# Kernel optimization log

Hardware: AMD Instinct MI355X
Metric: run time of the kernel (lower is better)

Reference implementation:

```python
import jax, jax.numpy as jnp
import numpy as np
import math

B, S, N_STATE = 2, 2048, 2048
N_HEAD, D_HEAD = 16, 128
NEG = -1e9


def rope(x, f_r, f_i):
    # x: [B,S,H,D], f_*: [B,S,1,D//2]
    x_r, x_i = jnp.split(x, 2, axis=-1)
    return jnp.concatenate([x_r * f_r - x_i * f_i, x_r * f_i + x_i * f_r], axis=-1)


def setup_inputs() -> dict:
    key = jax.random.key(0)
    ks = jax.random.split(key, 6)
    x = jax.random.normal(ks[0], (B, S, N_STATE), jnp.float32)
    # rotary freqs: cos/sin of standard RoPE angles
    inv_freq = 1.0 / (10000.0 ** (jnp.arange(0, D_HEAD, 2, dtype=jnp.float32) / D_HEAD))
    ang = jnp.arange(S, dtype=jnp.float32)[:, None] * inv_freq[None, :]  # [S, D/2]
    f_r = jnp.broadcast_to(jnp.cos(ang)[None, :, None, :], (B, S, 1, D_HEAD // 2))
    f_i = jnp.broadcast_to(jnp.sin(ang)[None, :, None, :], (B, S, 1, D_HEAD // 2))
    # causal additive mask: 0 on/below diagonal, -1e9 above
    causal = jnp.where(jnp.tril(jnp.ones((S, S), bool)), 0.0, NEG).astype(jnp.float32)
    attention_mask = jnp.broadcast_to(causal[None], (B, S, S))
    std = 1.0 / math.sqrt(N_STATE)
    W_qkv = jax.random.normal(ks[1], (3 * N_HEAD * D_HEAD, N_STATE), jnp.float32) * std
    b_qkv = jax.random.normal(ks[2], (3 * N_HEAD * D_HEAD,), jnp.float32) * 0.02
    W_o = jax.random.normal(ks[3], (N_STATE, N_HEAD * D_HEAD), jnp.float32) * std
    return {"x": x, "f_r": f_r, "f_i": f_i, "attention_mask": attention_mask,
            "W_qkv": W_qkv, "b_qkv": b_qkv, "W_o": W_o}


def reference(x, f_r, f_i, attention_mask, W_qkv, b_qkv, W_o):
    nb, ns, _ = x.shape
    qkv = x @ W_qkv.T + b_qkv  # [B,S,3*H*D]
    q, k, v = jnp.split(qkv, 3, axis=-1)
    q = rope(q.reshape(nb, ns, N_HEAD, D_HEAD), f_r, f_i)
    k = rope(k.reshape(nb, ns, N_HEAD, D_HEAD), f_r, f_i)
    v = v.reshape(nb, ns, N_HEAD, D_HEAD)
    # kv_cache=None: cache is just (k, v)
    qk = jnp.einsum("bqhd,bkhd->bhqk", q, k) / math.sqrt(D_HEAD)
    qk = qk + attention_mask[:, None, :, :]
    scores = jax.nn.softmax(qk.astype(jnp.float32), axis=-1).astype(x.dtype)
    out = jnp.einsum("bhqk,bkhd->bqhd", scores, v).reshape(nb, ns, N_HEAD * D_HEAD)
    out = out @ W_o.T
    return out, k, v
```

## Files before the change

kernel.cpp:

```cpp
#include <hip/hip_runtime.h>
#include <stdint.h>

#define BS   2
#define SS   2048
#define NH   16
#define DH   128
#define HD   2048
#define KDIM 2048
#define NT   32

typedef _Float16 half_t;
typedef _Float16 half8 __attribute__((ext_vector_type(8)));
typedef _Float16 half4v __attribute__((ext_vector_type(4)));
typedef float   float4_ __attribute__((ext_vector_type(4)));

__device__ __forceinline__ void async16(const void* g, void* l) {
  __builtin_amdgcn_global_load_lds(
      (__attribute__((address_space(1))) void*)(void*)g,
      (__attribute__((address_space(3))) void*)l,
      16, 0, 0);
}

__global__ __launch_bounds__(256) void f32_to_f16_k(const float* __restrict__ in,
                                                    half_t* __restrict__ out, int n4) {
  int i = blockIdx.x * 256 + threadIdx.x;
  if (i < n4) {
    float4 v = ((const float4*)in)[i];
    half4v h;
    h.x = (half_t)v.x; h.y = (half_t)v.y; h.z = (half_t)v.z; h.w = (half_t)v.w;
    ((half4v*)out)[i] = h;
  }
}


__device__ __forceinline__ const half8* lds_frag(const half_t* l, int row, int j) {
  return (const half8*)&l[(row * 8 + (j ^ (row & 7))) * 8];
}

__device__ __forceinline__ void stage8(const half_t* __restrict__ Ab,
                                       const half_t* __restrict__ Wb,
                                       half_t* dA, half_t* dB, int k0,
                                       int wave, int lane) {
#pragma unroll
  for (int i = 0; i < 4; ++i) {
    int p = (wave * 4 + i) * 64 + lane;
    int r = p >> 3, j = (p & 7) ^ ((p >> 3) & 7);
    async16(Ab + (size_t)r * KDIM + k0 + j * 8, &dA[p * 8]);
    async16(Wb + (size_t)r * KDIM + k0 + j * 8, &dB[p * 8]);
  }
}

__device__ __forceinline__ void gemm_core(const half_t* __restrict__ Ab,
                                          const half_t* __restrict__ Wb,
                                          half_t* lA, half_t* lB,
                                          float4_ acc[4][4]) {
  const int tid = threadIdx.x, wave = tid >> 6, lane = tid & 63;
  const int quad = lane >> 4, tl = lane & 15;
  const int wm = wave >> 1, wn = wave & 1;

  stage8(Ab, Wb, lA, lB, 0, wave, lane);
  stage8(Ab, Wb, lA + 8192, lB + 8192, 64, wave, lane);

  for (int t = 0; t < NT; ++t) {
    if (t == NT - 1) asm volatile("s_waitcnt vmcnt(0)" ::: "memory");
    else             asm volatile("s_waitcnt vmcnt(8)" ::: "memory");
    __builtin_amdgcn_s_barrier();

    const half_t* cA = lA + (t & 1) * 8192;
    const half_t* cB = lB + (t & 1) * 8192;
    half8 af[4][2], bf[4][2];
#pragma unroll
    for (int ks = 0; ks < 2; ++ks) {
#pragma unroll
      for (int mi = 0; mi < 4; ++mi)
        af[mi][ks] = *lds_frag(cA, wm * 64 + mi * 16 + tl, ks * 4 + quad);
#pragma unroll
      for (int ni = 0; ni < 4; ++ni)
        bf[ni][ks] = *lds_frag(cB, wn * 64 + ni * 16 + tl, ks * 4 + quad);
    }
    asm volatile("s_waitcnt lgkmcnt(0)" ::: "memory");
    __builtin_amdgcn_sched_barrier(0);
    __builtin_amdgcn_s_barrier();

    if (t + 2 < NT)
      stage8(Ab, Wb, lA + (t & 1) * 8192, lB + (t & 1) * 8192,
             (t + 2) * 64, wave, lane);
    __builtin_amdgcn_sched_barrier(0);

    __builtin_amdgcn_s_setprio(1);
#pragma unroll
    for (int mi = 0; mi < 4; ++mi)
#pragma unroll
      for (int ni = 0; ni < 4; ++ni)
#pragma unroll
        for (int ks = 0; ks < 2; ++ks)
          acc[mi][ni] = __builtin_amdgcn_mfma_f32_16x16x32_f16(
              af[mi][ks], bf[ni][ks], acc[mi][ni], 0, 0, 0);
    __builtin_amdgcn_s_setprio(0);
  }
}

__global__ __launch_bounds__(256) void gemm_qkv(const half_t* __restrict__ A,
                                                const half_t* __restrict__ W,
                                                const float* __restrict__ bias,
                                                half_t* __restrict__ qh,
                                                half_t* __restrict__ kh,
                                                half_t* __restrict__ vh,
                                                float* __restrict__ vout) {
  __shared__ __align__(16) half_t lA[2 * 128 * 64];
  __shared__ __align__(16) half_t lB[2 * 128 * 64];
  const int tid = threadIdx.x, wave = tid >> 6, lane = tid & 63;
  const int quad = lane >> 4, tl = lane & 15;
  const int wm = wave >> 1, wn = wave & 1;
  const int bm = blockIdx.y * 128, bn = blockIdx.x * 128;

  float4_ acc[4][4];
#pragma unroll
  for (int mi = 0; mi < 4; ++mi)
#pragma unroll
    for (int ni = 0; ni < 4; ++ni)
#pragma unroll
      for (int r = 0; r < 4; ++r) acc[mi][ni][r] = 0.f;

  gemm_core(A + (size_t)bm * KDIM, W + (size_t)bn * KDIM, lA, lB, acc);

#pragma unroll
  for (int mi = 0; mi < 4; ++mi) {
    int rowb = bm + wm * 64 + mi * 16 + quad * 4;
#pragma unroll
    for (int ni = 0; ni < 4; ++ni) {
      int col = bn + wn * 64 + ni * 16 + tl;
      float bv = bias[col];
#pragma unroll
      for (int r = 0; r < 4; ++r) {
        float v = acc[mi][ni][r] + bv;
        size_t off = (size_t)(rowb + r) * HD;
        if (col < 2048)       qh[off + col]        = (half_t)v;
        else if (col < 4096)  kh[off + col - 2048] = (half_t)v;
        else {
          vh[off + col - 4096]   = (half_t)v;
          vout[off + col - 4096] = v;
        }
      }
    }
  }
}

__global__ __launch_bounds__(256) void gemm_out(const half_t* __restrict__ A,
                                                const half_t* __restrict__ W,
                                                float* __restrict__ out) {
  __shared__ __align__(16) half_t lA[2 * 128 * 64];
  __shared__ __align__(16) half_t lB[2 * 128 * 64];
  const int tid = threadIdx.x, wave = tid >> 6, lane = tid & 63;
  const int quad = lane >> 4, tl = lane & 15;
  const int wm = wave >> 1, wn = wave & 1;
  const int bm = blockIdx.y * 128, bn = blockIdx.x * 128;

  float4_ acc[4][4];
#pragma unroll
  for (int mi = 0; mi < 4; ++mi)
#pragma unroll
    for (int ni = 0; ni < 4; ++ni)
#pragma unroll
      for (int r = 0; r < 4; ++r) acc[mi][ni][r] = 0.f;

  gemm_core(A + (size_t)bm * KDIM, W + (size_t)bn * KDIM, lA, lB, acc);

#pragma unroll
  for (int mi = 0; mi < 4; ++mi) {
    int rowb = bm + wm * 64 + mi * 16 + quad * 4;
#pragma unroll
    for (int ni = 0; ni < 4; ++ni) {
      int col = bn + wn * 64 + ni * 16 + tl;
#pragma unroll
      for (int r = 0; r < 4; ++r)
        out[(size_t)(rowb + r) * HD + col] = acc[mi][ni][r];
    }
  }
}

__global__ __launch_bounds__(256) void rope_post(half_t* __restrict__ qh,
                                                 half_t* __restrict__ kh,
                                                 const float* __restrict__ fr,
                                                 const float* __restrict__ fi,
                                                 float* __restrict__ kout) {
  int n = blockIdx.x * 256 + threadIdx.x;
  int u = n & 7;
  int h = (n >> 3) & 15;
  int s = (n >> 7) & 2047;
  int b = n >> 18;
  size_t row = (size_t)(b * SS + s);
  size_t base = row * HD + h * DH + u * 8;
  const float4_* fr4 = (const float4_*)(fr + row * 64 + u * 8);
  const float4_* fi4 = (const float4_*)(fi + row * 64 + u * 8);
  float4_ frv0 = fr4[0], frv1 = fr4[1];
  float4_ fiv0 = fi4[0], fiv1 = fi4[1];
  half8 qlo = *(const half8*)(qh + base), qhi = *(const half8*)(qh + base + 64);
  half8 klo = *(const half8*)(kh + base), khi = *(const half8*)(kh + base + 64);
  half8 qlo_o, qhi_o, klo_o, khi_o;
  float4_ kr0, kr1, ki0, ki1;
#pragma unroll
  for (int j = 0; j < 8; ++j) {
    float cr = (j < 4) ? frv0[j & 3] : frv1[j & 3];
    float ci = (j < 4) ? fiv0[j & 3] : fiv1[j & 3];
    float xr = (float)qlo[j], xi = (float)qhi[j];
    qlo_o[j] = (half_t)(xr * cr - xi * ci);
    qhi_o[j] = (half_t)(xr * ci + xi * cr);
    xr = (float)klo[j]; xi = (float)khi[j];
    float kr = xr * cr - xi * ci, ki = xr * ci + xi * cr;
    klo_o[j] = (half_t)kr; khi_o[j] = (half_t)ki;
    if (j < 4) { kr0[j & 3] = kr; ki0[j & 3] = ki; }
    else       { kr1[j & 3] = kr; ki1[j & 3] = ki; }
  }
  *(half8*)(qh + base)      = qlo_o;
  *(half8*)(qh + base + 64) = qhi_o;
  *(half8*)(kh + base)      = klo_o;
  *(half8*)(kh + base + 64) = khi_o;
  ((float4_*)(kout + base))[0]      = kr0;
  ((float4_*)(kout + base))[1]      = kr1;
  ((float4_*)(kout + base + 64))[0] = ki0;
  ((float4_*)(kout + base + 64))[1] = ki1;
}

__global__ __launch_bounds__(256) void vpost(const half_t* __restrict__ vh,
                                             half_t* __restrict__ vt) {
  __shared__ half_t t[64 * 66];
  int d0 = blockIdx.x * 64, s0 = blockIdx.y * 64, bh = blockIdx.z;
  int b = bh >> 4, h = bh & 15;
#pragma unroll
  for (int i = 0; i < 16; ++i) {
    int idx = i * 256 + threadIdx.x;
    int s = idx >> 6, d = idx & 63;
    size_t g = (size_t)(b * SS + s0 + s) * HD + h * DH + d0 + d;
    t[d * 66 + s] = vh[g];
  }
  __syncthreads();
#pragma unroll
  for (int i = 0; i < 16; ++i) {
    int idx = i * 256 + threadIdx.x;
    int d = idx >> 6, s = idx & 63;
    vt[((size_t)bh * DH + d0 + d) * SS + s0 + s] = t[d * 66 + s];
  }
}

#define SOFTMAX_SHIFT 2.0f

__device__ __forceinline__ void stage_kv(const half_t* __restrict__ khb,
                                         const half_t* __restrict__ vtb,
                                         half_t* dK, half_t* dV, int kt,
                                         int wave, int lane) {
#pragma unroll
  for (int i = 0; i < 4; ++i) {
    int p = (wave * 4 + i) * 64 + lane;
    int rk = p >> 4, jk = (p & 15) ^ ((p >> 4) & 7);
    async16(khb + (size_t)(kt * 64 + rk) * HD + jk * 8, &dK[p * 8]);
    int rv = p >> 3, jv = (p & 7) ^ ((p >> 3) & 7);
    async16(vtb + (size_t)rv * SS + kt * 64 + jv * 8, &dV[p * 8]);
  }
}

__global__ __launch_bounds__(256) void attn_kernel(const half_t* __restrict__ qh,
                                                   const half_t* __restrict__ kh,
                                                   const half_t* __restrict__ vt,
                                                   half_t* __restrict__ oh) {
  __shared__ __align__(16) half_t lK[2 * 64 * 128];
  __shared__ __align__(16) half_t lV[2 * 128 * 64];
  __shared__ __align__(16) half_t lP[4 * 16 * 72];
  const int bh = blockIdx.y;
  const int b = bh >> 4, h = bh & 15;
  const int tid = threadIdx.x, wave = tid >> 6, lane = tid & 63;
  const int quad = lane >> 4, tl = lane & 15;
  const float scale = 0.08838834764831845f;

  half_t* myP = &lP[wave * 16 * 72];
  const half_t* qbase = qh + (size_t)(b * SS) * HD + h * DH;
  const half_t* khb   = kh + (size_t)(b * SS) * HD + h * DH;
  const half_t* vtb   = vt + (size_t)bh * DH * SS;

  for (int ph = 0; ph < 2; ++ph) {
    const int qt = ph ? (31 - (int)blockIdx.x) : (int)blockIdx.x;
    const int q0 = qt * 64 + wave * 16;

    half8 qf[4];
#pragma unroll
    for (int ks = 0; ks < 4; ++ks)
      qf[ks] = *(const half8*)(qbase + (size_t)(q0 + tl) * HD + ks * 32 + quad * 8);

    float4_ oacc[8];
#pragma unroll
    for (int t = 0; t < 8; ++t)
#pragma unroll
      for (int r = 0; r < 4; ++r) oacc[t][r] = 0.f;
    float lpart[4] = {0.f, 0.f, 0.f, 0.f};

    stage_kv(khb, vtb, lK, lV, 0, wave, lane);

    for (int kt = 0; kt <= qt; ++kt) {
      const half_t* cK = lK + (kt & 1) * 8192;
      const half_t* cV = lV + (kt & 1) * 8192;
      if (kt < qt) {
        stage_kv(khb, vtb, lK + ((kt + 1) & 1) * 8192, lV + ((kt + 1) & 1) * 8192,
                 kt + 1, wave, lane);
        asm volatile("s_waitcnt vmcnt(8)" ::: "memory");
      } else {
        asm volatile("s_waitcnt vmcnt(0)" ::: "memory");
      }
      __builtin_amdgcn_s_barrier();
      __builtin_amdgcn_sched_barrier(0);

      float4_ sacc[4];
#pragma unroll
      for (int tn = 0; tn < 4; ++tn)
#pragma unroll
        for (int r = 0; r < 4; ++r) sacc[tn][r] = 0.f;
      __builtin_amdgcn_s_setprio(1);
#pragma unroll
      for (int ks = 0; ks < 4; ++ks) {
#pragma unroll
        for (int tn = 0; tn < 4; ++tn) {
          int row = tn * 16 + tl;
          int j = ks * 4 + quad;
          half8 kf = *(const half8*)&cK[(row * 16 + (j ^ (row & 7))) * 8];
          sacc[tn] = __builtin_amdgcn_mfma_f32_16x16x32_f16(qf[ks], kf, sacc[tn], 0, 0, 0);
        }
      }
      __builtin_amdgcn_s_setprio(0);

      if (kt == qt) {
#pragma unroll
        for (int tn = 0; tn < 4; ++tn) {
          int kvcol = kt * 64 + tn * 16 + tl;
#pragma unroll
          for (int j = 0; j < 4; ++j) {
            int qrow = q0 + quad * 4 + j;
            float sv = fmaf(sacc[tn][j], scale, -SOFTMAX_SHIFT);
            float pv = (kvcol > qrow) ? 0.f : __expf(sv);
            lpart[j] += pv;
            myP[(quad * 4 + j) * 72 + tn * 16 + tl] = (half_t)pv;
          }
        }
      } else {
#pragma unroll
        for (int tn = 0; tn < 4; ++tn)
#pragma unroll
          for (int j = 0; j < 4; ++j) {
            float pv = __expf(fmaf(sacc[tn][j], scale, -SOFTMAX_SHIFT));
            lpart[j] += pv;
            myP[(quad * 4 + j) * 72 + tn * 16 + tl] = (half_t)pv;
          }
      }

      __builtin_amdgcn_s_setprio(1);
#pragma unroll
      for (int ks2 = 0; ks2 < 2; ++ks2) {
        half8 pf = *(const half8*)&myP[tl * 72 + ks2 * 32 + quad * 8];
#pragma unroll
        for (int t = 0; t < 8; ++t) {
          int row = t * 16 + tl;
          int j = ks2 * 4 + quad;
          half8 vf = *(const half8*)&cV[(row * 8 + (j ^ (row & 7))) * 8];
          oacc[t] = __builtin_amdgcn_mfma_f32_16x16x32_f16(pf, vf, oacc[t], 0, 0, 0);
        }
      }
      __builtin_amdgcn_s_setprio(0);
      __builtin_amdgcn_s_barrier();
    }

#pragma unroll
    for (int off = 1; off <= 8; off <<= 1)
#pragma unroll
      for (int j = 0; j < 4; ++j)
        lpart[j] += __shfl_xor(lpart[j], off, 64);
    float inv[4];
#pragma unroll
    for (int j = 0; j < 4; ++j) inv[j] = 1.f / lpart[j];
#pragma unroll
    for (int t = 0; t < 8; ++t)
#pragma unroll
      for (int j = 0; j < 4; ++j)
        oh[(size_t)(b * SS + q0 + quad * 4 + j) * HD + h * DH + t * 16 + tl] =
            (half_t)(oacc[t][j] * inv[j]);
  }
}

extern "C" void kernel_launch(void* const* d_in, const int* in_sizes, int n_in,
                              void* d_out, int out_size, void* d_ws, size_t ws_size,
                              hipStream_t stream) {
  const float* x    = (const float*)d_in[0];
  const float* fr   = (const float*)d_in[1];
  const float* fi   = (const float*)d_in[2];
  const float* Wqkv = (const float*)d_in[4];
  const float* bqkv = (const float*)d_in[5];
  const float* Wo   = (const float*)d_in[6];

  float* out  = (float*)d_out;
  float* kout = out + 8388608;
  float* vout = out + 16777216;

  char* ws = (char*)d_ws;
  half_t* xh  = (half_t*)(ws);
  half_t* wqh = (half_t*)(ws + 16777216);
  half_t* woh = (half_t*)(ws + 41943040);
  half_t* qh  = (half_t*)(ws + 50331648);
  half_t* kh  = (half_t*)(ws + 67108864);
  half_t* vh  = (half_t*)(ws + 83886080);
  half_t* vt  = (half_t*)(ws + 100663296);
  half_t* oh  = (half_t*)(ws + 117440512);

  f32_to_f16_k<<<8192, 256, 0, stream>>>(x, xh, 2097152);
  f32_to_f16_k<<<12288, 256, 0, stream>>>(Wqkv, wqh, 3145728);
  f32_to_f16_k<<<4096, 256, 0, stream>>>(Wo, woh, 1048576);
  gemm_qkv<<<dim3(48, 32), 256, 0, stream>>>(xh, wqh, bqkv, qh, kh, vh, vout);
  rope_post<<<2048, 256, 0, stream>>>(qh, kh, fr, fi, kout);
  vpost<<<dim3(2, 32, 32), 256, 0, stream>>>(vh, vt);
  attn_kernel<<<dim3(16, 32), 256, 0, stream>>>(qh, kh, vt, oh);
  gemm_out<<<dim3(16, 32), 256, 0, stream>>>(oh, woh, out);
}
```

Baseline: 453.5 us.

## Fuse conversions, vectorize V transpose, drop LDS staging in attention

Measured after the change: 816.8 us. +80.1%, slower.

```diff
diff --git a/kernel.cpp b/kernel.cpp
--- a/kernel.cpp
+++ b/kernel.cpp
@@ -21,15 +21,24 @@
       16, 0, 0);
 }
 
-__global__ __launch_bounds__(256) void f32_to_f16_k(const float* __restrict__ in,
-                                                    half_t* __restrict__ out, int n4) {
+#define XN4  2097152
+#define WQ4  3145728
+#define WO4  1048576
+__global__ __launch_bounds__(256) void conv_all(const float* __restrict__ x,
+                                                const float* __restrict__ Wqkv,
+                                                const float* __restrict__ Wo,
+                                                half_t* __restrict__ xh,
+                                                half_t* __restrict__ wqh,
+                                                half_t* __restrict__ woh) {
   int i = blockIdx.x * 256 + threadIdx.x;
-  if (i < n4) {
-    float4 v = ((const float4*)in)[i];
-    half4v h;
-    h.x = (half_t)v.x; h.y = (half_t)v.y; h.z = (half_t)v.z; h.w = (half_t)v.w;
-    ((half4v*)out)[i] = h;
-  }
+  const float* src; half_t* dst; int o;
+  if (i < XN4)            { src = x;    dst = xh;  o = i; }
+  else if (i < XN4 + WQ4) { src = Wqkv; dst = wqh; o = i - XN4; }
+  else                    { src = Wo;   dst = woh; o = i - XN4 - WQ4; }
+  float4 v = ((const float4*)src)[o];
+  half4v hv;
+  hv.x = (half_t)v.x; hv.y = (half_t)v.y; hv.z = (half_t)v.z; hv.w = (half_t)v.w;
+  ((half4v*)dst)[o] = hv;
 }
 
 
@@ -224,47 +233,35 @@
 
 __global__ __launch_bounds__(256) void vpost(const half_t* __restrict__ vh,
                                              half_t* __restrict__ vt) {
-  __shared__ half_t t[64 * 66];
+  __shared__ half_t t[64 * 72];
   int d0 = blockIdx.x * 64, s0 = blockIdx.y * 64, bh = blockIdx.z;
   int b = bh >> 4, h = bh & 15;
 #pragma unroll
-  for (int i = 0; i < 16; ++i) {
-    int idx = i * 256 + threadIdx.x;
-    int s = idx >> 6, d = idx & 63;
-    size_t g = (size_t)(b * SS + s0 + s) * HD + h * DH + d0 + d;
-    t[d * 66 + s] = vh[g];
+  for (int it = 0; it < 2; ++it) {
+    int e = it * 256 + threadIdx.x;
+    int s = e >> 3, du = e & 7;
+    half8 v = *(const half8*)(vh + (size_t)(b * SS + s0 + s) * HD + h * DH + d0 + du * 8);
+#pragma unroll
+    for (int j = 0; j < 8; ++j) t[(du * 8 + j) * 72 + s] = v[j];
   }
   __syncthreads();
 #pragma unroll
-  for (int i = 0; i < 16; ++i) {
-    int idx = i * 256 + threadIdx.x;
-    int d = idx >> 6, s = idx & 63;
-    vt[((size_t)bh * DH + d0 + d) * SS + s0 + s] = t[d * 66 + s];
+  for (int it = 0; it < 2; ++it) {
+    int e = it * 256 + threadIdx.x;
+    int d = e >> 3, su = e & 7;
+    half8 v;
+#pragma unroll
+    for (int j = 0; j < 8; ++j) v[j] = t[d * 72 + su * 8 + j];
+    *(half8*)(vt + ((size_t)bh * DH + d0 + d) * SS + s0 + su * 8) = v;
   }
 }
 
 #define SOFTMAX_SHIFT 2.0f
 
-__device__ __forceinline__ void stage_kv(const half_t* __restrict__ khb,
-                                         const half_t* __restrict__ vtb,
-                                         half_t* dK, half_t* dV, int kt,
-                                         int wave, int lane) {
-#pragma unroll
-  for (int i = 0; i < 4; ++i) {
-    int p = (wave * 4 + i) * 64 + lane;
-    int rk = p >> 4, jk = (p & 15) ^ ((p >> 4) & 7);
-    async16(khb + (size_t)(kt * 64 + rk) * HD + jk * 8, &dK[p * 8]);
-    int rv = p >> 3, jv = (p & 7) ^ ((p >> 3) & 7);
-    async16(vtb + (size_t)rv * SS + kt * 64 + jv * 8, &dV[p * 8]);
-  }
-}
-
-__global__ __launch_bounds__(256) void attn_kernel(const half_t* __restrict__ qh,
-                                                   const half_t* __restrict__ kh,
-                                                   const half_t* __restrict__ vt,
-                                                   half_t* __restrict__ oh) {
-  __shared__ __align__(16) half_t lK[2 * 64 * 128];
-  __shared__ __align__(16) half_t lV[2 * 128 * 64];
+__global__ __launch_bounds__(256, 3) void attn_kernel(const half_t* __restrict__ qh,
+                                                      const half_t* __restrict__ kh,
+                                                      const half_t* __restrict__ vt,
+                                                      half_t* __restrict__ oh) {
   __shared__ __align__(16) half_t lP[4 * 16 * 72];
   const int bh = blockIdx.y;
   const int b = bh >> 4, h = bh & 15;
@@ -277,110 +274,87 @@
   const half_t* khb   = kh + (size_t)(b * SS) * HD + h * DH;
   const half_t* vtb   = vt + (size_t)bh * DH * SS;
 
-  for (int ph = 0; ph < 2; ++ph) {
-    const int qt = ph ? (31 - (int)blockIdx.x) : (int)blockIdx.x;
-    const int q0 = qt * 64 + wave * 16;
-
-    half8 qf[4];
-#pragma unroll
-    for (int ks = 0; ks < 4; ++ks)
-      qf[ks] = *(const half8*)(qbase + (size_t)(q0 + tl) * HD + ks * 32 + quad * 8);
-
-    float4_ oacc[8];
-#pragma unroll
-    for (int t = 0; t < 8; ++t)
-#pragma unroll
-      for (int r = 0; r < 4; ++r) oacc[t][r] = 0.f;
-    float lpart[4] = {0.f, 0.f, 0.f, 0.f};
-
-    stage_kv(khb, vtb, lK, lV, 0, wave, lane);
-
-    for (int kt = 0; kt <= qt; ++kt) {
-      const half_t* cK = lK + (kt & 1) * 8192;
-      const half_t* cV = lV + (kt & 1) * 8192;
-      if (kt < qt) {
-        stage_kv(khb, vtb, lK + ((kt + 1) & 1) * 8192, lV + ((kt + 1) & 1) * 8192,
-                 kt + 1, wave, lane);
-        asm volatile("s_waitcnt vmcnt(8)" ::: "memory");
-      } else {
-        asm volatile("s_waitcnt vmcnt(0)" ::: "memory");
+  const int qt = 31 - (int)blockIdx.x;
+  const int q0 = qt * 64 + wave * 16;
+
+  half8 qf[4];
+#pragma unroll
+  for (int ks = 0; ks < 4; ++ks)
+    qf[ks] = *(const half8*)(qbase + (size_t)(q0 + tl) * HD + ks * 32 + quad * 8);
+
+  float4_ oacc[8];
+#pragma unroll
+  for (int t = 0; t < 8; ++t)
+#pragma unroll
+    for (int r = 0; r < 4; ++r) oacc[t][r] = 0.f;
+  float lpart[4] = {0.f, 0.f, 0.f, 0.f};
+
+  for (int kt = 0; kt <= qt; ++kt) {
+    float4_ sacc[4];
+#pragma unroll
+    for (int tn = 0; tn < 4; ++tn)
+#pragma unroll
+      for (int r = 0; r < 4; ++r) sacc[tn][r] = 0.f;
+#pragma unroll
+    for (int ks = 0; ks < 4; ++ks) {
+#pragma unroll
+      for (int tn = 0; tn < 4; ++tn) {
+        half8 kf = *(const half8*)(khb + (size_t)(kt * 64 + tn * 16 + tl) * HD +
+                                   ks * 32 + quad * 8);
+        sacc[tn] = __builtin_amdgcn_mfma_f32_16x16x32_f16(qf[ks], kf, sacc[tn], 0, 0, 0);
       }
-      __builtin_amdgcn_s_barrier();
-      __builtin_amdgcn_sched_barrier(0);
-
-      float4_ sacc[4];
-#pragma unroll
-      for (int tn = 0; tn < 4; ++tn)
-#pragma unroll
-        for (int r = 0; r < 4; ++r) sacc[tn][r] = 0.f;
-      __builtin_amdgcn_s_setprio(1);
-#pragma unroll
-      for (int ks = 0; ks < 4; ++ks) {
-#pragma unroll
-        for (int tn = 0; tn < 4; ++tn) {
-          int row = tn * 16 + tl;
-          int j = ks * 4 + quad;
-          half8 kf = *(const half8*)&cK[(row * 16 + (j ^ (row & 7))) * 8];
-          sacc[tn] = __builtin_amdgcn_mfma_f32_16x16x32_f16(qf[ks], kf, sacc[tn], 0, 0, 0);
+    }
+
+    if (kt == qt) {
+#pragma unroll
+      for (int tn = 0; tn < 4; ++tn) {
+        int kvcol = kt * 64 + tn * 16 + tl;
+#pragma unroll
+        for (int j = 0; j < 4; ++j) {
+          int qrow = q0 + quad * 4 + j;
+          float sv = fmaf(sacc[tn][j], scale, -SOFTMAX_SHIFT);
+          float pv = (kvcol > qrow) ? 0.f : __expf(sv);
+          lpart[j] += pv;
+          myP[(quad * 4 + j) * 72 + tn * 16 + tl] = (half_t)pv;
         }
       }
-      __builtin_amdgcn_s_setprio(0);
-
-      if (kt == qt) {
-#pragma unroll
-        for (int tn = 0; tn < 4; ++tn) {
-          int kvcol = kt * 64 + tn * 16 + tl;
-#pragma unroll
-          for (int j = 0; j < 4; ++j) {
-            int qrow = q0 + quad * 4 + j;
-            float sv = fmaf(sacc[tn][j], scale, -SOFTMAX_SHIFT);
-            float pv = (kvcol > qrow) ? 0.f : __expf(sv);
-            lpart[j] += pv;
-            myP[(quad * 4 + j) * 72 + tn * 16 + tl] = (half_t)pv;
-          }
+    } else {
+#pragma unroll
+      for (int tn = 0; tn < 4; ++tn)
+#pragma unroll
+        for (int j = 0; j < 4; ++j) {
+          float pv = __expf(fmaf(sacc[tn][j], scale, -SOFTMAX_SHIFT));
+          lpart[j] += pv;
+          myP[(quad * 4 + j) * 72 + tn * 16 + tl] = (half_t)pv;
         }
-      } else {
-#pragma unroll
-        for (int tn = 0; tn < 4; ++tn)
-#pragma unroll
-          for (int j = 0; j < 4; ++j) {
-            float pv = __expf(fmaf(sacc[tn][j], scale, -SOFTMAX_SHIFT));
-            lpart[j] += pv;
-            myP[(quad * 4 + j) * 72 + tn * 16 + tl] = (half_t)pv;
-          }
+    }
+
+#pragma unroll
+    for (int ks2 = 0; ks2 < 2; ++ks2) {
+      half8 pf = *(const half8*)&myP[tl * 72 + ks2 * 32 + quad * 8];
+#pragma unroll
+      for (int t = 0; t < 8; ++t) {
+        half8 vf = *(const half8*)(vtb + (size_t)(t * 16 + tl) * SS + kt * 64 +
+                                   ks2 * 32 + quad * 8);
+        oacc[t] = __builtin_amdgcn_mfma_f32_16x16x32_f16(pf, vf, oacc[t], 0, 0, 0);
       }
-
-      __builtin_amdgcn_s_setprio(1);
-#pragma unroll
-      for (int ks2 = 0; ks2 < 2; ++ks2) {
-        half8 pf = *(const half8*)&myP[tl * 72 + ks2 * 32 + quad * 8];
-#pragma unroll
-        for (int t = 0; t < 8; ++t) {
-          int row = t * 16 + tl;
-          int j = ks2 * 4 + quad;
-          half8 vf = *(const half8*)&cV[(row * 8 + (j ^ (row & 7))) * 8];
-          oacc[t] = __builtin_amdgcn_mfma_f32_16x16x32_f16(pf, vf, oacc[t], 0, 0, 0);
-        }
-      }
-      __builtin_amdgcn_s_setprio(0);
-      __builtin_amdgcn_s_barrier();
-    }
-
-#pragma unroll
-    for (int off = 1; off <= 8; off <<= 1)
-#pragma unroll
-      for (int j = 0; j < 4; ++j)
-        lpart[j] += __shfl_xor(lpart[j], off, 64);
-    float inv[4];
-#pragma unroll
-    for (int j = 0; j < 4; ++j) inv[j] = 1.f / lpart[j];
-#pragma unroll
-    for (int t = 0; t < 8; ++t)
-#pragma unroll
-      for (int j = 0; j < 4; ++j)
-        oh[(size_t)(b * SS + q0 + quad * 4 + j) * HD + h * DH + t * 16 + tl] =
-            (half_t)(oacc[t][j] * inv[j]);
-  }
+    }
+  }
+
+#pragma unroll
+  for (int off = 1; off <= 8; off <<= 1)
+#pragma unroll
+    for (int j = 0; j < 4; ++j)
+      lpart[j] += __shfl_xor(lpart[j], off, 64);
+  float inv[4];
+#pragma unroll
+  for (int j = 0; j < 4; ++j) inv[j] = 1.f / lpart[j];
+#pragma unroll
+  for (int t = 0; t < 8; ++t)
+#pragma unroll
+    for (int j = 0; j < 4; ++j)
+      oh[(size_t)(b * SS + q0 + quad * 4 + j) * HD + h * DH + t * 16 + tl] =
+          (half_t)(oacc[t][j] * inv[j]);
 }
 
 extern "C" void kernel_launch(void* const* d_in, const int* in_sizes, int n_in,
@@ -407,12 +381,10 @@
   half_t* vt  = (half_t*)(ws + 100663296);
   half_t* oh  = (half_t*)(ws + 117440512);
 
-  f32_to_f16_k<<<8192, 256, 0, stream>>>(x, xh, 2097152);
-  f32_to_f16_k<<<12288, 256, 0, stream>>>(Wqkv, wqh, 3145728);
-  f32_to_f16_k<<<4096, 256, 0, stream>>>(Wo, woh, 1048576);
+  conv_all<<<24576, 256, 0, stream>>>(x, Wqkv, Wo, xh, wqh, woh);
   gemm_qkv<<<dim3(48, 32), 256, 0, stream>>>(xh, wqh, bqkv, qh, kh, vh, vout);
   rope_post<<<2048, 256, 0, stream>>>(qh, kh, fr, fi, kout);
   vpost<<<dim3(2, 32, 32), 256, 0, stream>>>(vh, vt);
-  attn_kernel<<<dim3(16, 32), 256, 0, stream>>>(qh, kh, vt, oh);
+  attn_kernel<<<dim3(32, 32), 256, 0, stream>>>(qh, kh, vt, oh);
   gemm_out<<<dim3(16, 32), 256, 0, stream>>>(oh, woh, out);
 }
```
